# Performance work log

Measured on AMD Instinct MI355X. Metric: run time of the kernel, lower is better.

## Reference

```python
import jax, jax.numpy as jnp
import numpy as np


def setup_inputs() -> dict:
    key = jax.random.key(0)
    kq, kk, kv = jax.random.split(key, 3)
    B, S, D = 16, 2048, 128
    q = jax.random.normal(kq, (B, S, D), dtype=jnp.float32)
    k = jax.random.normal(kk, (B, S, D), dtype=jnp.float32)
    v = jax.random.normal(kv, (B, S, D), dtype=jnp.float32)
    return {"q": q, "k": k, "v": v}


def reference(q, k, v):
    # scores: [B, Sq, Sk] = q @ k^T, scaled by 1/sqrt(D)
    scale = k.shape[-1] ** -0.5
    scores = jnp.einsum("bqd,bkd->bqk", q, k) * scale
    attention = jax.nn.softmax(scores, axis=2)  # Softmax(dim=2)
    # dropout p=0.0 -> identity (eval-mode equivalent)
    context = jnp.einsum("bqk,bkd->bqd", attention, v)
    return (context, attention)
```

## Files before the change

kernel.cpp:

```cpp
#include <hip/hip_runtime.h>
#include <stdint.h>

#define BB 16
#define SS 2048
#define DD 128

typedef __attribute__((ext_vector_type(8))) short short8;
typedef __attribute__((ext_vector_type(4))) short short4v;
typedef __attribute__((ext_vector_type(4))) float float4v;

__device__ __forceinline__ short f2b(float f){
  unsigned u = __float_as_uint(f);
  u += 0x7fffu + ((u >> 16) & 1u);
  return (short)(u >> 16);
}
__device__ __forceinline__ float b2f(short h){
  return __uint_as_float(((unsigned)(unsigned short)h) << 16);
}

__global__ __launch_bounds__(256) void cvt_k(const float* __restrict__ k, short* __restrict__ kb){
  int i = blockIdx.x * 256 + threadIdx.x;
  float4v f = ((const float4v*)k)[i];
  short4v h;
  h[0]=f2b(f[0]); h[1]=f2b(f[1]); h[2]=f2b(f[2]); h[3]=f2b(f[3]);
  ((short4v*)kb)[i] = h;
}

__global__ __launch_bounds__(256) void trans_v(const float* __restrict__ v, short* __restrict__ vt){
  __shared__ float tile[32][33];
  int blk = blockIdx.x;
  int b   = blk >> 8;
  int rem = blk & 255;
  int k0 = (rem >> 2) << 5;
  int d0 = (rem & 3) << 5;
  int r = threadIdx.x >> 5, c = threadIdx.x & 31;
  const float* vb = v + (size_t)b * SS * DD;
  #pragma unroll
  for (int i=0;i<4;i++)
    tile[r + 8*i][c] = vb[(size_t)(k0 + r + 8*i) * DD + d0 + c];
  __syncthreads();
  short* vtb = vt + (size_t)b * DD * SS;
  #pragma unroll
  for (int i=0;i<4;i++)
    vtb[(size_t)(d0 + r + 8*i) * SS + k0 + c] = f2b(tile[c][r + 8*i]);
}

__global__ __launch_bounds__(512) void attn(const float* __restrict__ q,
                                            const short* __restrict__ kb,
                                            const short* __restrict__ vt,
                                            float* __restrict__ out){
  __shared__ __align__(16) short Pt[16 * 2056];
  __shared__ __align__(16) short KV[128 * 136];
  __shared__ float lpart[512];
  __shared__ float invl[16];

  const float scale = 0.08838834764831845f;
  int blk = blockIdx.x;
  int b   = blk >> 7;
  int q0  = (blk & 127) << 4;
  int tid = threadIdx.x;
  int w    = tid >> 6;
  int L    = tid & 63;
  int m    = L & 15;
  int quad = L >> 4;

  short8 aq[4];
  {
    const float* qrow = q + (size_t)(b * SS + q0 + m) * DD;
    #pragma unroll
    for (int fi=0; fi<4; fi++){
      int d0 = fi*32 + quad*8;
      short8 h;
      #pragma unroll
      for (int j=0;j<8;j++) h[j] = f2b(qrow[d0 + j]);
      aq[fi] = h;
    }
  }

  const short* kbB = kb + (size_t)b * SS * DD;
  int lw = w << 4;

  for (int kt=0; kt<16; kt++){
    int k0 = kt << 7;
    __syncthreads();
    #pragma unroll
    for (int i=0;i<4;i++){
      int g = tid + (i << 9);
      int key = g >> 4;
      int c8  = (g & 15) << 3;
      *(short8*)&KV[key*136 + c8] = *(const short8*)(kbB + (size_t)(k0 + key)*DD + c8);
    }
    __syncthreads();

    const short* krow = &KV[(lw + m) * 136];
    short8 b0 = *(const short8*)(krow + quad*8);
    short8 b1 = *(const short8*)(krow + 32 + quad*8);
    short8 b2 = *(const short8*)(krow + 64 + quad*8);
    short8 b3 = *(const short8*)(krow + 96 + quad*8);
    float4v a0 = {0.f,0.f,0.f,0.f}, a1 = {0.f,0.f,0.f,0.f};
    a0 = __builtin_amdgcn_mfma_f32_16x16x32_bf16(aq[0], b0, a0, 0,0,0);
    a1 = __builtin_amdgcn_mfma_f32_16x16x32_bf16(aq[1], b1, a1, 0,0,0);
    a0 = __builtin_amdgcn_mfma_f32_16x16x32_bf16(aq[2], b2, a0, 0,0,0);
    a1 = __builtin_amdgcn_mfma_f32_16x16x32_bf16(aq[3], b3, a1, 0,0,0);

    int col = k0 + lw + m;
    #pragma unroll
    for (int r=0;r<4;r++){
      float p = __expf((a0[r] + a1[r]) * scale);
      Pt[(quad*4 + r) * 2056 + col] = f2b(p);
    }
  }

  __syncthreads();
  {
    int row = tid >> 5, seg = tid & 31;
    const short* pr = &Pt[row * 2056 + seg * 64];
    float s = 0.f;
    #pragma unroll
    for (int i=0;i<64;i++) s += b2f(pr[i]);
    lpart[tid] = s;
  }
  __syncthreads();
  if (tid < 16){
    float s = 0.f;
    #pragma unroll
    for (int j=0;j<32;j++) s += lpart[tid*32 + j];
    invl[tid] = 1.0f / s;
  }
  __syncthreads();

  float* ctx = out;
  float* att = out + (size_t)BB * SS * DD;
  float* attBase = att + (size_t)(b * SS + q0) * SS;

  const short* vtB = vt + (size_t)b * DD * SS;
  float4v o0 = {0.f,0.f,0.f,0.f}, o1 = {0.f,0.f,0.f,0.f};

  for (int kt=0; kt<16; kt++){
    int k0 = kt << 7;
    __syncthreads();
    #pragma unroll
    for (int i=0;i<4;i++){
      int g = tid + (i << 9);
      int d  = g >> 4;
      int c8 = (g & 15) << 3;
      *(short8*)&KV[d*136 + c8] = *(const short8*)(vtB + (size_t)d * SS + k0 + c8);
    }
    __syncthreads();

    {
      int row = tid >> 5;
      int c4  = (tid & 31) << 2;
      short4v h = *(const short4v*)&Pt[row * 2056 + k0 + c4];
      float il = invl[row];
      float4v f;
      f[0] = b2f(h[0]) * il; f[1] = b2f(h[1]) * il;
      f[2] = b2f(h[2]) * il; f[3] = b2f(h[3]) * il;
      *(float4v*)(attBase + (size_t)row * SS + k0 + c4) = f;
    }

    const short* vrow = &KV[(lw + m) * 136];
    #pragma unroll
    for (int kk=0; kk<4; kk++){
      short8 af = *(const short8*)&Pt[m * 2056 + k0 + kk*32 + quad*8];
      short8 bf = *(const short8*)(vrow + kk*32 + quad*8);
      if (kk & 1) o1 = __builtin_amdgcn_mfma_f32_16x16x32_bf16(af, bf, o1, 0,0,0);
      else        o0 = __builtin_amdgcn_mfma_f32_16x16x32_bf16(af, bf, o0, 0,0,0);
    }
  }

  #pragma unroll
  for (int r=0;r<4;r++){
    int row = quad*4 + r;
    ctx[(size_t)(b * SS + q0 + row) * DD + lw + m] = (o0[r] + o1[r]) * invl[row];
  }
}

extern "C" void kernel_launch(void* const* d_in, const int* in_sizes, int n_in,
                              void* d_out, int out_size, void* d_ws, size_t ws_size,
                              hipStream_t stream) {
  const float* q = (const float*)d_in[0];
  const float* k = (const float*)d_in[1];
  const float* v = (const float*)d_in[2];
  float* out = (float*)d_out;
  short* kbf = (short*)d_ws;
  short* vtr = kbf + (size_t)BB * SS * DD;
  cvt_k  <<<(BB*SS*DD/4)/256, 256, 0, stream>>>(k, kbf);
  trans_v<<<BB*(SS/32)*(DD/32), 256, 0, stream>>>(v, vtr);
  attn   <<<BB*(SS/16), 512, 0, stream>>>(q, kbf, vtr, out);
}
```

Measured before the change: 532.9 us.

## Drop LDS staging of K/V, fuse row sums, swizzle blocks, nontemporal stores

Removes the shared-memory staging buffer for K and V tiles, so each lane reads its MFMA B fragments directly from global memory. This eliminates per-tile barriers and cuts LDS to about 66KB, which together with the launch_bounds occupancy hint allows more resident blocks per CU. Row sums for softmax are now accumulated in registers during the exp pass and reduced with wave shuffles, replacing the later LDS re-scan. Blocks are swizzled so that consecutive block IDs spread across batches, and the large attention-matrix and context outputs are written with nontemporal stores. The risk is that direct global fragment loads are less coalesced and depend on L2/cache hits for reuse across waves.

```diff
diff --git a/kernel.cpp b/kernel.cpp
--- a/kernel.cpp
+++ b/kernel.cpp
@@ -45,24 +45,25 @@
     vtb[(size_t)(d0 + r + 8*i) * SS + k0 + c] = f2b(tile[c][r + 8*i]);
 }
 
-__global__ __launch_bounds__(512) void attn(const float* __restrict__ q,
-                                            const short* __restrict__ kb,
-                                            const short* __restrict__ vt,
-                                            float* __restrict__ out){
+__global__ __launch_bounds__(512, 4) void attn(const float* __restrict__ q,
+                                               const short* __restrict__ kb,
+                                               const short* __restrict__ vt,
+                                               float* __restrict__ out){
   __shared__ __align__(16) short Pt[16 * 2056];
-  __shared__ __align__(16) short KV[128 * 136];
-  __shared__ float lpart[512];
+  __shared__ float red[8][16];
   __shared__ float invl[16];
 
   const float scale = 0.08838834764831845f;
   int blk = blockIdx.x;
-  int b   = blk >> 7;
-  int q0  = (blk & 127) << 4;
+  int swz = ((blk & 7) << 8) + (blk >> 3);
+  int b   = swz >> 7;
+  int q0  = (swz & 127) << 4;
   int tid = threadIdx.x;
   int w    = tid >> 6;
   int L    = tid & 63;
   int m    = L & 15;
   int quad = L >> 4;
+  int lw   = w << 4;
 
   short8 aq[4];
   {
@@ -78,25 +79,15 @@
   }
 
   const short* kbB = kb + (size_t)b * SS * DD;
-  int lw = w << 4;
 
+  float rs[4] = {0.f, 0.f, 0.f, 0.f};
   for (int kt=0; kt<16; kt++){
     int k0 = kt << 7;
-    __syncthreads();
-    #pragma unroll
-    for (int i=0;i<4;i++){
-      int g = tid + (i << 9);
-      int key = g >> 4;
-      int c8  = (g & 15) << 3;
-      *(short8*)&KV[key*136 + c8] = *(const short8*)(kbB + (size_t)(k0 + key)*DD + c8);
-    }
-    __syncthreads();
-
-    const short* krow = &KV[(lw + m) * 136];
-    short8 b0 = *(const short8*)(krow + quad*8);
-    short8 b1 = *(const short8*)(krow + 32 + quad*8);
-    short8 b2 = *(const short8*)(krow + 64 + quad*8);
-    short8 b3 = *(const short8*)(krow + 96 + quad*8);
+    const short* kg = kbB + (size_t)(k0 + lw + m) * DD + quad*8;
+    short8 b0 = *(const short8*)(kg);
+    short8 b1 = *(const short8*)(kg + 32);
+    short8 b2 = *(const short8*)(kg + 64);
+    short8 b3 = *(const short8*)(kg + 96);
     float4v a0 = {0.f,0.f,0.f,0.f}, a1 = {0.f,0.f,0.f,0.f};
     a0 = __builtin_amdgcn_mfma_f32_16x16x32_bf16(aq[0], b0, a0, 0,0,0);
     a1 = __builtin_amdgcn_mfma_f32_16x16x32_bf16(aq[1], b1, a1, 0,0,0);
@@ -107,24 +98,30 @@
     #pragma unroll
     for (int r=0;r<4;r++){
       float p = __expf((a0[r] + a1[r]) * scale);
-      Pt[(quad*4 + r) * 2056 + col] = f2b(p);
+      short h = f2b(p);
+      rs[r] += b2f(h);
+      Pt[(quad*4 + r) * 2056 + col] = h;
     }
   }
 
-  __syncthreads();
-  {
-    int row = tid >> 5, seg = tid & 31;
-    const short* pr = &Pt[row * 2056 + seg * 64];
-    float s = 0.f;
+  #pragma unroll
+  for (int r=0;r<4;r++){
+    float s = rs[r];
+    s += __shfl_xor(s, 1);
+    s += __shfl_xor(s, 2);
+    s += __shfl_xor(s, 4);
+    s += __shfl_xor(s, 8);
+    rs[r] = s;
+  }
+  if (m == 0){
     #pragma unroll
-    for (int i=0;i<64;i++) s += b2f(pr[i]);
-    lpart[tid] = s;
+    for (int r=0;r<4;r++) red[w][quad*4 + r] = rs[r];
   }
   __syncthreads();
   if (tid < 16){
     float s = 0.f;
     #pragma unroll
-    for (int j=0;j<32;j++) s += lpart[tid*32 + j];
+    for (int j=0;j<8;j++) s += red[j][tid];
     invl[tid] = 1.0f / s;
   }
   __syncthreads();
@@ -132,38 +129,28 @@
   float* ctx = out;
   float* att = out + (size_t)BB * SS * DD;
   float* attBase = att + (size_t)(b * SS + q0) * SS;
+  const short* vtB = vt + (size_t)b * DD * SS;
 
-  const short* vtB = vt + (size_t)b * DD * SS;
   float4v o0 = {0.f,0.f,0.f,0.f}, o1 = {0.f,0.f,0.f,0.f};
+  int row2 = tid >> 5;
+  int c4   = (tid & 31) << 2;
+  float il2 = 0.f;
+  const short* vg = vtB + (size_t)(lw + m) * SS + quad*8;
 
   for (int kt=0; kt<16; kt++){
     int k0 = kt << 7;
-    __syncthreads();
-    #pragma unroll
-    for (int i=0;i<4;i++){
-      int g = tid + (i << 9);
-      int d  = g >> 4;
-      int c8 = (g & 15) << 3;
-      *(short8*)&KV[d*136 + c8] = *(const short8*)(vtB + (size_t)d * SS + k0 + c8);
+    {
+      short4v h = *(const short4v*)&Pt[row2 * 2056 + k0 + c4];
+      il2 = invl[row2];
+      float4v f;
+      f[0] = b2f(h[0]) * il2; f[1] = b2f(h[1]) * il2;
+      f[2] = b2f(h[2]) * il2; f[3] = b2f(h[3]) * il2;
+      __builtin_nontemporal_store(f, (float4v*)(attBase + (size_t)row2 * SS + k0 + c4));
     }
-    __syncthreads();
-
-    {
-      int row = tid >> 5;
-      int c4  = (tid & 31) << 2;
-      short4v h = *(const short4v*)&Pt[row * 2056 + k0 + c4];
-      float il = invl[row];
-      float4v f;
-      f[0] = b2f(h[0]) * il; f[1] = b2f(h[1]) * il;
-      f[2] = b2f(h[2]) * il; f[3] = b2f(h[3]) * il;
-      *(float4v*)(attBase + (size_t)row * SS + k0 + c4) = f;
-    }
-
-    const short* vrow = &KV[(lw + m) * 136];
     #pragma unroll
     for (int kk=0; kk<4; kk++){
       short8 af = *(const short8*)&Pt[m * 2056 + k0 + kk*32 + quad*8];
-      short8 bf = *(const short8*)(vrow + kk*32 + quad*8);
+      short8 bf = *(const short8*)(vg + k0 + kk*32);
       if (kk & 1) o1 = __builtin_amdgcn_mfma_f32_16x16x32_bf16(af, bf, o1, 0,0,0);
       else        o0 = __builtin_amdgcn_mfma_f32_16x16x32_bf16(af, bf, o0, 0,0,0);
     }
@@ -172,7 +159,8 @@
   #pragma unroll
   for (int r=0;r<4;r++){
     int row = quad*4 + r;
-    ctx[(size_t)(b * SS + q0 + row) * DD + lw + m] = (o0[r] + o1[r]) * invl[row];
+    __builtin_nontemporal_store((o0[r] + o1[r]) * invl[row],
+                                &ctx[(size_t)(b * SS + q0 + row) * DD + lw + m]);
   }
 }
 
```

Result: faster. 515.9 us (-3.2%).
